# Optimization experiments

Measured on AMD Instinct MI355X. Metric: run time of the kernel, lower is better.

The kernel has to match this reference:

```python
import jax, jax.numpy as jnp
import numpy as np


def setup_inputs() -> dict:
    key = jax.random.key(0)
    ks = jax.random.split(key, 4)
    B, S, D, U = 4, 4096, 128, 64
    x = jax.random.normal(ks[0], (B, S, D), dtype=jnp.float32)
    Wq = jax.random.normal(ks[1], (D, U), dtype=jnp.float32) * (1.0 / np.sqrt(D))
    Wk = jax.random.normal(ks[2], (D, U), dtype=jnp.float32) * (1.0 / np.sqrt(D))
    Wv = jax.random.normal(ks[3], (D, U), dtype=jnp.float32) * (1.0 / np.sqrt(D))
    bq = jnp.zeros((U,), dtype=jnp.float32)
    bk = jnp.zeros((U,), dtype=jnp.float32)
    bv = jnp.zeros((U,), dtype=jnp.float32)
    return {"x": x, "Wq": Wq, "bq": bq, "Wk": Wk, "bk": bk, "Wv": Wv, "bv": bv}


def reference(x, Wq, bq, Wk, bk, Wv, bv):
    # Single-head, unscaled, unmasked attention (faithful to the Keras layer).
    q = jnp.einsum("bsd,du->bsu", x, Wq) + bq  # [B,S,U]
    k = jnp.einsum("bsd,du->bsu", x, Wk) + bk  # [B,S,U]
    v = jnp.einsum("bsd,du->bsu", x, Wv) + bv  # [B,S,U]
    scores = jnp.einsum("bsu,btu->bst", q, k)  # [B,S,S], no 1/sqrt(d) scaling
    attn = jax.nn.softmax(scores, axis=-1)
    return jnp.einsum("bst,btu->bsu", attn, v)  # [B,S,U]
```

## Files before the change

### kernel.cpp

```cpp
#include <hip/hip_runtime.h>
#include <hip/hip_fp16.h>
#include <math.h>

#define SEQ   4096
#define DIM   128
#define UDIM  64
#define BATCH 4
#define BS    (BATCH*SEQ)

typedef _Float16 h8 __attribute__((ext_vector_type(8)));
typedef _Float16 h4 __attribute__((ext_vector_type(4)));
typedef _Float16 h2 __attribute__((ext_vector_type(2)));
typedef float    f4 __attribute__((ext_vector_type(4)));

#define MFMA_K32(a,b,c) __builtin_amdgcn_mfma_f32_16x16x32_f16((a),(b),(c),0,0,0)
#define MFMA_K16(a,b,c) __builtin_amdgcn_mfma_f32_16x16x16f16((a),(b),(c),0,0,0)

__device__ __forceinline__ h2 pk2(float a, float b) {
  return __builtin_bit_cast(h2, __builtin_amdgcn_cvt_pkrtz(a, b));
}

#define WT_STRIDE 272
#define VB_STRIDE 144
#define L2E 1.44269504088896f

__global__ __launch_bounds__(256, 3) void proj_mfma(
    const float* __restrict__ x,
    const float* __restrict__ Wq, const float* __restrict__ bq,
    const float* __restrict__ Wk, const float* __restrict__ bk,
    const float* __restrict__ Wv, const float* __restrict__ bv,
    _Float16* __restrict__ qf, _Float16* __restrict__ kf, _Float16* __restrict__ vt)
{
  const int proj = blockIdx.y;
  const float* __restrict__ W    = proj==0 ? Wq : (proj==1 ? Wk : Wv);
  const float* __restrict__ bias = proj==0 ? bq : (proj==1 ? bk : bv);
  const int tid  = threadIdx.x;
  const int lane = tid & 63, wv = tid >> 6;
  const int n = lane & 15, quad = lane >> 4;
  const int r0 = blockIdx.x * 64;

  __shared__ __align__(16) char lds[UDIM * WT_STRIDE];

  #pragma unroll
  for (int i = 0; i < 8; ++i) {
    const int idx = i*256 + tid;
    const int nn  = idx & 63;
    const int k4  = (idx >> 6) * 4;
    const float w0 = W[(k4+0)*UDIM + nn];
    const float w1 = W[(k4+1)*UDIM + nn];
    const float w2 = W[(k4+2)*UDIM + nn];
    const float w3 = W[(k4+3)*UDIM + nn];
    int2 wd;
    wd.x = __builtin_bit_cast(int, pk2(w0, w1));
    wd.y = __builtin_bit_cast(int, pk2(w2, w3));
    *(int2*)(lds + nn*WT_STRIDE + k4*2) = wd;
  }
  __syncthreads();

  const int row = r0 + wv*16 + n;
  h8 xa[4];
  #pragma unroll
  for (int ks = 0; ks < 4; ++ks) {
    const float* xp = x + (size_t)row*DIM + ks*32 + quad*8;
    const f4 a = *(const f4*)xp, b = *(const f4*)(xp + 4);
    int4 pkd;
    pkd.x = __builtin_bit_cast(int, pk2(a[0], a[1]));
    pkd.y = __builtin_bit_cast(int, pk2(a[2], a[3]));
    pkd.z = __builtin_bit_cast(int, pk2(b[0], b[1]));
    pkd.w = __builtin_bit_cast(int, pk2(b[2], b[3]));
    xa[ks] = __builtin_bit_cast(h8, pkd);
  }

  f4 acc[4];
  #pragma unroll
  for (int nt = 0; nt < 4; ++nt) acc[nt] = (f4){0.f,0.f,0.f,0.f};

  #pragma unroll
  for (int ks = 0; ks < 4; ++ks)
    #pragma unroll
    for (int nt = 0; nt < 4; ++nt) {
      const h8 wf = *(const h8*)(lds + (nt*16 + n)*WT_STRIDE + (ks*32 + quad*8)*2);
      acc[nt] = MFMA_K32(xa[ks], wf, acc[nt]);
    }

  #pragma unroll
  for (int nt = 0; nt < 4; ++nt) {
    const float bb = bias[nt*16 + n];
    #pragma unroll
    for (int r = 0; r < 4; ++r) acc[nt][r] += bb;
  }

  if (proj < 2) {
    _Float16* __restrict__ out = (proj == 0) ? qf : kf;
    const int par = lane & 1;
    const unsigned sel = par ? 0x03020706u : 0x05040100u;
    #pragma unroll
    for (int nt = 0; nt < 4; ++nt)
      #pragma unroll
      for (int p = 0; p < 2; ++p) {
        const int r = 2*p;
        unsigned A  = __builtin_bit_cast(unsigned, pk2(acc[nt][r], acc[nt][r+1]));
        unsigned Bs = (unsigned)__builtin_amdgcn_mov_dpp((int)A, 0xB1, 0xF, 0xF, true);
        unsigned w  = __builtin_amdgcn_perm(Bs, A, sel);
        const int orow = r0 + wv*16 + 4*quad + r + par;
        const int ocol = nt*16 + n - par;
        *(unsigned*)((char*)out + ((size_t)orow*UDIM + ocol)*2) = w;
      }
  } else {
    __syncthreads();
    #pragma unroll
    for (int nt = 0; nt < 4; ++nt)
      #pragma unroll
      for (int p = 0; p < 2; ++p) {
        const int r = 2*p;
        const int u = nt*16 + n;
        const int lrow = wv*16 + 4*quad + r;
        *(unsigned*)(lds + u*VB_STRIDE + lrow*2) =
            __builtin_bit_cast(unsigned, pk2(acc[nt][r], acc[nt][r+1]));
      }
    __syncthreads();
    const int b  = r0 / SEQ;
    const int s0 = r0 % SEQ;
    #pragma unroll
    for (int i = 0; i < 2; ++i) {
      const int e = tid + 256*i;
      const int u = e >> 3, ch = e & 7;
      h8 v = *(const h8*)(lds + u*VB_STRIDE + ch*16);
      *(h8*)(vt + ((size_t)b*UDIM + u)*SEQ + s0 + ch*8) = v;
    }
  }
}

__global__ __launch_bounds__(256, 3) void flash_attn_t(
    const _Float16* __restrict__ qf, const _Float16* __restrict__ kf,
    const _Float16* __restrict__ vt,
    _Float16* __restrict__ opart, float* __restrict__ Mp, float* __restrict__ Lp,
    int nkt)
{
  const int qt = blockIdx.x, b = blockIdx.y, sp = blockIdx.z;
  const _Float16* __restrict__ qb = qf + (size_t)b*SEQ*UDIM;
  const _Float16* __restrict__ kb = kf + (size_t)b*SEQ*UDIM;
  const _Float16* __restrict__ vb = vt + (size_t)b*UDIM*SEQ;

  __shared__ __align__(16) char Ks[64 * VB_STRIDE];
  __shared__ __align__(16) char Vs[64 * VB_STRIDE];

  const int tid = threadIdx.x;
  const int lane = tid & 63, wv = tid >> 6;
  const int n = lane & 15, quad = lane >> 4;
  const int qbase = qt*128 + wv*32;

  h8 qB[2][2];
  #pragma unroll
  for (int nt = 0; nt < 2; ++nt)
    #pragma unroll
    for (int ks = 0; ks < 2; ++ks)
      qB[nt][ks] = *(const h8*)(qb + (size_t)(qbase + nt*16 + n)*UDIM + ks*32 + quad*8);

  f4 O[4][2];
  #pragma unroll
  for (int ut = 0; ut < 4; ++ut)
    #pragma unroll
    for (int nt = 0; nt < 2; ++nt) O[ut][nt] = (f4){0.f,0.f,0.f,0.f};

  float M[2] = {-1e30f, -1e30f};
  float Ls[2] = {0.f, 0.f};

  const int e4a = tid, e4b = tid + 256;
  const _Float16* kga = kb + ((size_t)(sp*nkt)*64 + (e4a>>3))*UDIM + (e4a&7)*8;
  const _Float16* kgb = kb + ((size_t)(sp*nkt)*64 + (e4b>>3))*UDIM + (e4b&7)*8;
  const _Float16* vga = vb + (size_t)(e4a>>3)*SEQ + sp*nkt*64 + (e4a&7)*8;
  const _Float16* vgb = vb + (size_t)(e4b>>3)*SEQ + sp*nkt*64 + (e4b&7)*8;
  char* kda = Ks + (e4a>>3)*VB_STRIDE + (e4a&7)*16;
  char* kdb = Ks + (e4b>>3)*VB_STRIDE + (e4b&7)*16;
  char* vda = Vs + (e4a>>3)*VB_STRIDE + (e4a&7)*16;
  char* vdb = Vs + (e4b>>3)*VB_STRIDE + (e4b&7)*16;

  for (int kt = 0; kt < nkt; ++kt) {
    __syncthreads();
    *(h8*)kda = *(const h8*)kga;  kga += (size_t)64*UDIM;
    *(h8*)kdb = *(const h8*)kgb;  kgb += (size_t)64*UDIM;
    *(h8*)vda = *(const h8*)vga;  vga += 64;
    *(h8*)vdb = *(const h8*)vgb;  vgb += 64;
    __syncthreads();

    f4 S[4][2];
    #pragma unroll
    for (int mt = 0; mt < 4; ++mt)
      #pragma unroll
      for (int nt = 0; nt < 2; ++nt) S[mt][nt] = (f4){0.f,0.f,0.f,0.f};

    #pragma unroll
    for (int ks = 0; ks < 2; ++ks) {
      h8 ka[4];
      #pragma unroll
      for (int mt = 0; mt < 4; ++mt)
        ka[mt] = *(const h8*)(Ks + (mt*16 + n)*VB_STRIDE + ks*64 + quad*16);
      #pragma unroll
      for (int mt = 0; mt < 4; ++mt)
        #pragma unroll
        for (int nt = 0; nt < 2; ++nt)
          S[mt][nt] = MFMA_K32(ka[mt], qB[nt][ks], S[mt][nt]);
    }

    float alpha[2];
    #pragma unroll
    for (int nt = 0; nt < 2; ++nt) {
      float rm = S[0][nt][0];
      #pragma unroll
      for (int mt = 0; mt < 4; ++mt)
        #pragma unroll
        for (int r = 0; r < 4; ++r) rm = fmaxf(rm, S[mt][nt][r]);
      rm = fmaxf(rm, __shfl_xor(rm, 16));
      rm = fmaxf(rm, __shfl_xor(rm, 32));
      const float mo = M[nt];
      const float mn = fmaxf(mo, rm);
      alpha[nt] = exp2f((mo - mn) * L2E);
      const float mnl = mn * L2E;
      float rs = 0.f;
      #pragma unroll
      for (int mt = 0; mt < 4; ++mt)
        #pragma unroll
        for (int r = 0; r < 4; ++r) {
          const float p = exp2f(fmaf(S[mt][nt][r], L2E, -mnl));
          S[mt][nt][r] = p;
          rs += p;
        }
      rs += __shfl_xor(rs, 16);
      rs += __shfl_xor(rs, 32);
      M[nt]  = mn;
      Ls[nt] = Ls[nt] * alpha[nt] + rs;
      #pragma unroll
      for (int ut = 0; ut < 4; ++ut)
        #pragma unroll
        for (int r = 0; r < 4; ++r) O[ut][nt][r] *= alpha[nt];
    }

    h4 pB[4][2];
    #pragma unroll
    for (int mt = 0; mt < 4; ++mt)
      #pragma unroll
      for (int nt = 0; nt < 2; ++nt) {
        int2 t;
        t.x = __builtin_bit_cast(int, pk2(S[mt][nt][0], S[mt][nt][1]));
        t.y = __builtin_bit_cast(int, pk2(S[mt][nt][2], S[mt][nt][3]));
        pB[mt][nt] = __builtin_bit_cast(h4, t);
      }

    #pragma unroll
    for (int mt = 0; mt < 4; ++mt) {
      h4 va[4];
      #pragma unroll
      for (int ut = 0; ut < 4; ++ut)
        va[ut] = *(const h4*)(Vs + (ut*16 + n)*VB_STRIDE + mt*32 + quad*8);
      #pragma unroll
      for (int ut = 0; ut < 4; ++ut)
        #pragma unroll
        for (int nt = 0; nt < 2; ++nt)
          O[ut][nt] = MFMA_K16(va[ut], pB[mt][nt], O[ut][nt]);
    }
  }

  const size_t rowg = (size_t)sp*BS + (size_t)b*SEQ + qbase;
  #pragma unroll
  for (int nt = 0; nt < 2; ++nt) {
    char* __restrict__ orow = (char*)(opart + (rowg + nt*16 + n)*UDIM);
    #pragma unroll
    for (int ut = 0; ut < 4; ++ut)
      #pragma unroll
      for (int p = 0; p < 2; ++p)
        *(unsigned*)(orow + (ut*16 + quad*4 + 2*p)*2) =
            __builtin_bit_cast(unsigned, pk2(O[ut][nt][2*p], O[ut][nt][2*p+1]));
    if (quad == 0) {
      Mp[rowg + nt*16 + n] = M[nt] * L2E;
      Lp[rowg + nt*16 + n] = Ls[nt];
    }
  }
}

__global__ __launch_bounds__(256) void merge_out(
    const _Float16* __restrict__ opart, const float* __restrict__ Mp,
    const float* __restrict__ Lp, float* __restrict__ out, int nsplit)
{
  const int tid = threadIdx.x;
  const int row = blockIdx.x*16 + (tid >> 4);
  const int u4  = (tid & 15) * 4;
  float M = -1e30f;
  for (int s = 0; s < nsplit; ++s) M = fmaxf(M, Mp[(size_t)s*BS + row]);
  f4 num = (f4){0.f,0.f,0.f,0.f};
  float den = 0.f;
  for (int s = 0; s < nsplit; ++s) {
    const float w = exp2f(Mp[(size_t)s*BS + row] - M);
    den += w * Lp[(size_t)s*BS + row];
    const h4 op = *(const h4*)(opart + ((size_t)s*BS + row)*UDIM + u4);
    #pragma unroll
    for (int i = 0; i < 4; ++i) num[i] += w * (float)op[i];
  }
  const float dinv = 1.f / den;
  *(f4*)(out + (size_t)row*UDIM + u4) = num * dinv;
}

extern "C" void kernel_launch(void* const* d_in, const int* in_sizes, int n_in,
                              void* d_out, int out_size, void* d_ws, size_t ws_size,
                              hipStream_t stream) {
  (void)in_sizes; (void)n_in; (void)out_size;
  const float* x  = (const float*)d_in[0];
  const float* Wq = (const float*)d_in[1];
  const float* bq = (const float*)d_in[2];
  const float* Wk = (const float*)d_in[3];
  const float* bk = (const float*)d_in[4];
  const float* Wv = (const float*)d_in[5];
  const float* bv = (const float*)d_in[6];
  float* out = (float*)d_out;

  char* ws = (char*)d_ws;
  const size_t fBytes = (size_t)BS * UDIM * 2;
  auto need = [](int nsp) {
    return (size_t)3*BS*UDIM*2 + (size_t)nsp*BS*4*2 + (size_t)nsp*BS*UDIM*2;
  };
  int nsplit;
  if      (ws_size >= need(8)) nsplit = 8;
  else if (ws_size >= need(4)) nsplit = 4;
  else if (ws_size >= need(2)) nsplit = 2;
  else                         nsplit = 1;

  _Float16* qf = (_Float16*)(ws);
  _Float16* kf = (_Float16*)(ws + fBytes);
  _Float16* vt = (_Float16*)(ws + 2*fBytes);
  float* Mp    = (float*)(ws + 3*fBytes);
  float* Lp    = (float*)(ws + 3*fBytes + (size_t)nsplit*BS*4);
  _Float16* opart = (_Float16*)(ws + 3*fBytes + (size_t)nsplit*BS*8);

  proj_mfma<<<dim3(BS/64, 3), 256, 0, stream>>>(x, Wq, bq, Wk, bk, Wv, bv, qf, kf, vt);
  flash_attn_t<<<dim3(SEQ/128, BATCH, nsplit), 256, 0, stream>>>(
      qf, kf, vt, opart, Mp, Lp, (SEQ/64)/nsplit);
  merge_out<<<dim3(BS/16), 256, 0, stream>>>(opart, Mp, Lp, out, nsplit);
}
```

Measured before the change: 123.1 us.

## Double-buffer K/V tiles with register prefetch and compute row sums via MFMA

Loads the next K/V tile into registers before computing on the current LDS buffer, then stores it to the alternate buffer with a single barrier per iteration instead of two. Also replaces the scalar softmax row-sum and cross-lane shuffles with an extra MFMA against a ones vector. This doubles LDS footprint and adds MFMA work and register pressure in exchange for hiding global load latency.

```diff
diff --git a/kernel.cpp b/kernel.cpp
--- a/kernel.cpp
+++ b/kernel.cpp
@@ -142,8 +142,8 @@
   const _Float16* __restrict__ kb = kf + (size_t)b*SEQ*UDIM;
   const _Float16* __restrict__ vb = vt + (size_t)b*UDIM*SEQ;
 
-  __shared__ __align__(16) char Ks[64 * VB_STRIDE];
-  __shared__ __align__(16) char Vs[64 * VB_STRIDE];
+  __shared__ __align__(16) char Ks[2][64 * VB_STRIDE];
+  __shared__ __align__(16) char Vs[2][64 * VB_STRIDE];
 
   const int tid = threadIdx.x;
   const int lane = tid & 63, wv = tid >> 6;
@@ -157,32 +157,46 @@
     for (int ks = 0; ks < 2; ++ks)
       qB[nt][ks] = *(const h8*)(qb + (size_t)(qbase + nt*16 + n)*UDIM + ks*32 + quad*8);
 
-  f4 O[4][2];
+  f4 O[4][2], Ol[2];
   #pragma unroll
   for (int ut = 0; ut < 4; ++ut)
     #pragma unroll
     for (int nt = 0; nt < 2; ++nt) O[ut][nt] = (f4){0.f,0.f,0.f,0.f};
+  Ol[0] = (f4){0.f,0.f,0.f,0.f};
+  Ol[1] = (f4){0.f,0.f,0.f,0.f};
 
   float M[2] = {-1e30f, -1e30f};
-  float Ls[2] = {0.f, 0.f};
-
-  const int e4a = tid, e4b = tid + 256;
-  const _Float16* kga = kb + ((size_t)(sp*nkt)*64 + (e4a>>3))*UDIM + (e4a&7)*8;
-  const _Float16* kgb = kb + ((size_t)(sp*nkt)*64 + (e4b>>3))*UDIM + (e4b&7)*8;
-  const _Float16* vga = vb + (size_t)(e4a>>3)*SEQ + sp*nkt*64 + (e4a&7)*8;
-  const _Float16* vgb = vb + (size_t)(e4b>>3)*SEQ + sp*nkt*64 + (e4b&7)*8;
-  char* kda = Ks + (e4a>>3)*VB_STRIDE + (e4a&7)*16;
-  char* kdb = Ks + (e4b>>3)*VB_STRIDE + (e4b&7)*16;
-  char* vda = Vs + (e4a>>3)*VB_STRIDE + (e4a&7)*16;
-  char* vdb = Vs + (e4b>>3)*VB_STRIDE + (e4b&7)*16;
+
+  h4 ones_a;
+  { const _Float16 o = (_Float16)1.0f;
+    ones_a[0]=o; ones_a[1]=o; ones_a[2]=o; ones_a[3]=o; }
+
+  const int e0 = tid, e1 = tid + 256;
+  const _Float16* kg0 = kb + ((size_t)sp*nkt*64 + (e0>>3))*UDIM + (e0&7)*8;
+  const _Float16* kg1 = kb + ((size_t)sp*nkt*64 + (e1>>3))*UDIM + (e1&7)*8;
+  const _Float16* vg0 = vb + (size_t)(e0>>3)*SEQ + sp*nkt*64 + (e0&7)*8;
+  const _Float16* vg1 = vb + (size_t)(e1>>3)*SEQ + sp*nkt*64 + (e1&7)*8;
+  const int kofs0 = (e0>>3)*VB_STRIDE + (e0&7)*16;
+  const int kofs1 = (e1>>3)*VB_STRIDE + (e1&7)*16;
+
+  h8 pk0 = *(const h8*)kg0, pk1 = *(const h8*)kg1;
+  h8 pv0 = *(const h8*)vg0, pv1 = *(const h8*)vg1;
+  *(h8*)(Ks[0]+kofs0) = pk0;  *(h8*)(Ks[0]+kofs1) = pk1;
+  *(h8*)(Vs[0]+kofs0) = pv0;  *(h8*)(Vs[0]+kofs1) = pv1;
+  __syncthreads();
 
   for (int kt = 0; kt < nkt; ++kt) {
-    __syncthreads();
-    *(h8*)kda = *(const h8*)kga;  kga += (size_t)64*UDIM;
-    *(h8*)kdb = *(const h8*)kgb;  kgb += (size_t)64*UDIM;
-    *(h8*)vda = *(const h8*)vga;  vga += 64;
-    *(h8*)vdb = *(const h8*)vgb;  vgb += 64;
-    __syncthreads();
+    const int cur = kt & 1;
+    const bool more = (kt + 1 < nkt);
+    const char* __restrict__ Kc = Ks[cur];
+    const char* __restrict__ Vc = Vs[cur];
+
+    if (more) {
+      kg0 += (size_t)64*UDIM;  kg1 += (size_t)64*UDIM;
+      vg0 += 64;               vg1 += 64;
+      pk0 = *(const h8*)kg0;   pk1 = *(const h8*)kg1;
+      pv0 = *(const h8*)vg0;   pv1 = *(const h8*)vg1;
+    }
 
     f4 S[4][2];
     #pragma unroll
@@ -195,7 +209,7 @@
       h8 ka[4];
       #pragma unroll
       for (int mt = 0; mt < 4; ++mt)
-        ka[mt] = *(const h8*)(Ks + (mt*16 + n)*VB_STRIDE + ks*64 + quad*16);
+        ka[mt] = *(const h8*)(Kc + (mt*16 + n)*VB_STRIDE + ks*64 + quad*16);
       #pragma unroll
       for (int mt = 0; mt < 4; ++mt)
         #pragma unroll
@@ -217,23 +231,18 @@
       const float mn = fmaxf(mo, rm);
       alpha[nt] = exp2f((mo - mn) * L2E);
       const float mnl = mn * L2E;
-      float rs = 0.f;
       #pragma unroll
       for (int mt = 0; mt < 4; ++mt)
         #pragma unroll
-        for (int r = 0; r < 4; ++r) {
-          const float p = exp2f(fmaf(S[mt][nt][r], L2E, -mnl));
-          S[mt][nt][r] = p;
-          rs += p;
-        }
-      rs += __shfl_xor(rs, 16);
-      rs += __shfl_xor(rs, 32);
-      M[nt]  = mn;
-      Ls[nt] = Ls[nt] * alpha[nt] + rs;
+        for (int r = 0; r < 4; ++r)
+          S[mt][nt][r] = exp2f(fmaf(S[mt][nt][r], L2E, -mnl));
+      M[nt] = mn;
       #pragma unroll
       for (int ut = 0; ut < 4; ++ut)
         #pragma unroll
         for (int r = 0; r < 4; ++r) O[ut][nt][r] *= alpha[nt];
+      #pragma unroll
+      for (int r = 0; r < 4; ++r) Ol[nt][r] *= alpha[nt];
     }
 
     h4 pB[4][2];
@@ -252,12 +261,23 @@
       h4 va[4];
       #pragma unroll
       for (int ut = 0; ut < 4; ++ut)
-        va[ut] = *(const h4*)(Vs + (ut*16 + n)*VB_STRIDE + mt*32 + quad*8);
+        va[ut] = *(const h4*)(Vc + (ut*16 + n)*VB_STRIDE + mt*32 + quad*8);
       #pragma unroll
       for (int ut = 0; ut < 4; ++ut)
         #pragma unroll
         for (int nt = 0; nt < 2; ++nt)
           O[ut][nt] = MFMA_K16(va[ut], pB[mt][nt], O[ut][nt]);
+      #pragma unroll
+      for (int nt = 0; nt < 2; ++nt)
+        Ol[nt] = MFMA_K16(ones_a, pB[mt][nt], Ol[nt]);
+    }
+
+    if (more) {
+      char* __restrict__ Kn = Ks[cur ^ 1];
+      char* __restrict__ Vn = Vs[cur ^ 1];
+      *(h8*)(Kn+kofs0) = pk0;  *(h8*)(Kn+kofs1) = pk1;
+      *(h8*)(Vn+kofs0) = pv0;  *(h8*)(Vn+kofs1) = pv1;
+      __syncthreads();
     }
   }
 
@@ -273,7 +293,7 @@
             __builtin_bit_cast(unsigned, pk2(O[ut][nt][2*p], O[ut][nt][2*p+1]));
     if (quad == 0) {
       Mp[rowg + nt*16 + n] = M[nt] * L2E;
-      Lp[rowg + nt*16 + n] = Ls[nt];
+      Lp[rowg + nt*16 + n] = Ol[nt][0];
     }
   }
 }
```

Result: no change. 121.1 us (-1.7%).
